# Performance work log

Measured on AMD Instinct MI355X. Metric: run time of the kernel, lower is better.

## Reference

```python
import jax, jax.numpy as jnp
import numpy as np
from jax import lax

B, CIN, H, W = 8, 3, 256, 256
CMID = 16          # conv out channels == config.in_channels
DM = 256           # d_model
P = 2              # patch size (hardcoded in Downsample)
DI = 512           # d_inner = expand * d_model
NH, HD, NS, KC = 8, 64, 128, 4   # heads, headdim, d_state, d_conv
CONVDIM = DI + 2 * NS            # 768
PROJ = 2 * DI + 2 * NS + NH      # 1288


def _sincos2d(dim, gs):
    # 2d sin-cos positional embedding, matches get_2d_sincos_pos_embed
    def emb1d(d, pos):
        omega = 1.0 / (10000.0 ** (jnp.arange(d // 2, dtype=jnp.float32) / (d / 2.0)))
        out = pos[:, None] * omega[None, :]
        return jnp.concatenate([jnp.sin(out), jnp.cos(out)], axis=1)
    g = jnp.arange(gs, dtype=jnp.float32)
    grid = jnp.stack(jnp.meshgrid(g, g), 0).reshape(2, -1)  # [2, gs*gs]
    return jnp.concatenate([emb1d(dim // 2, grid[0]), emb1d(dim // 2, grid[1])], 1)


def _mamba2(u, in_proj_w, conv1d_w, conv1d_b, dt_bias, A_log, D, norm_w, out_proj_w):
    b, l, _ = u.shape
    zxbcdt = jnp.einsum('bld,pd->blp', u, in_proj_w)              # [b,l,1288]
    z = zxbcdt[..., :DI]
    xBC = zxbcdt[..., DI:DI + CONVDIM]
    dt = zxbcdt[..., DI + CONVDIM:]                                # [b,l,NH]
    # causal depthwise conv1d over sequence, then SiLU
    xc = lax.conv_general_dilated(xBC.transpose(0, 2, 1), conv1d_w, (1,), [(KC - 1, 0)],
                                  feature_group_count=CONVDIM,
                                  dimension_numbers=('NCH', 'OIH', 'NCH'))
    xBC = jax.nn.silu(xc + conv1d_b[None, :, None]).transpose(0, 2, 1)
    xh = xBC[..., :DI].reshape(b, l, NH, HD)                       # [b,l,h,p]
    Bm = xBC[..., DI:DI + NS]                                      # [b,l,n]
    Cm = xBC[..., DI + NS:]                                        # [b,l,n]
    dt = jax.nn.softplus(dt + dt_bias)                             # [b,l,h]
    dA = jnp.exp(dt * (-jnp.exp(A_log)))                           # [b,l,h]
    dtx = dt[..., None] * xh                                       # [b,l,h,p]

    def step(s, inp):
        dtx_t, B_t, C_t, dA_t = inp
        s = s * dA_t[..., None, None] + dtx_t[..., None] * B_t[:, None, None, :]
        return s, jnp.einsum('bhpn,bn->bhp', s, C_t)

    s0 = jnp.zeros((b, NH, HD, NS), u.dtype)
    _, ys = lax.scan(step, s0, (dtx.transpose(1, 0, 2, 3), Bm.transpose(1, 0, 2),
                                Cm.transpose(1, 0, 2), dA.transpose(1, 0, 2)))
    y = ys.transpose(1, 0, 2, 3) + D[None, None, :, None] * xh     # [b,l,h,p]
    y = y.reshape(b, l, DI) * jax.nn.silu(z)                       # gated
    y = y * lax.rsqrt(jnp.mean(y * y, -1, keepdims=True) + 1e-5) * norm_w
    return jnp.einsum('bld,od->blo', y, out_proj_w)


def setup_inputs() -> dict:
    key = jax.random.key(0)
    ks = jax.random.split(key, 12)
    r = lambda i, s, sc: jax.random.normal(ks[i], s, jnp.float32) * sc
    return {
        'x': jax.random.normal(ks[0], (B, CIN, H, W), jnp.float32),
        'conv_w': r(1, (CMID, CIN, 3, 3), 0.1), 'conv_b': jnp.zeros((CMID,), jnp.float32),
        'bn_gamma': jnp.ones((CMID,), jnp.float32), 'bn_beta': jnp.zeros((CMID,), jnp.float32),
        'patch_w': r(2, (DM, CMID, P, P), 0.1), 'patch_b': jnp.zeros((DM,), jnp.float32),
        'in_proj_w': r(3, (PROJ, DM), 0.02),
        'conv1d_w': r(4, (CONVDIM, 1, KC), 0.1), 'conv1d_b': jnp.zeros((CONVDIM,), jnp.float32),
        'dt_bias': r(5, (NH,), 0.5),
        'A_log': jax.random.uniform(ks[6], (NH,), jnp.float32),
        'D': jnp.ones((NH,), jnp.float32),
        'norm_w': jnp.ones((DI,), jnp.float32),
        'out_proj_w': r(7, (DM, DI), 0.02),
        'final_w': r(8, (P * P * CMID, DM), 0.02), 'final_b': jnp.zeros((P * P * CMID,), jnp.float32),
    }


def reference(x, conv_w, conv_b, bn_gamma, bn_beta, patch_w, patch_b, in_proj_w,
              conv1d_w, conv1d_b, dt_bias, A_log, D, norm_w, out_proj_w, final_w, final_b):
    # Conv2d k=3 s=2 p=1 -> BatchNorm2d (training-mode batch stats) -> GELU
    h = lax.conv_general_dilated(x, conv_w, (2, 2), [(1, 1), (1, 1)],
                                 dimension_numbers=('NCHW', 'OIHW', 'NCHW')) + conv_b[None, :, None, None]
    mu = jnp.mean(h, (0, 2, 3), keepdims=True)
    var = jnp.var(h, (0, 2, 3), keepdims=True)
    h = (h - mu) * lax.rsqrt(var + 1e-5) * bn_gamma[None, :, None, None] + bn_beta[None, :, None, None]
    h = jax.nn.gelu(h, approximate=False)
    # PatchEmbed: conv k=p s=p, flatten to tokens, add frozen sincos pos embed
    t = lax.conv_general_dilated(h, patch_w, (P, P), 'VALID',
                                 dimension_numbers=('NCHW', 'OIHW', 'NCHW')) + patch_b[None, :, None, None]
    b, d, gh, gw = t.shape
    tok = t.reshape(b, d, gh * gw).transpose(0, 2, 1) + _sincos2d(DM, gh)[None]
    # MambaBlock: Mamba2(x) + x  (layers=1; repo loop discards all but last layer)
    y = _mamba2(tok, in_proj_w, conv1d_w, conv1d_b, dt_bias, A_log, D, norm_w, out_proj_w) + tok
    # FinalLayer: linear only (norm_final is unused in its forward)
    o = jnp.einsum('bld,od->blo', y, final_w) + final_b
    # unpatchify
    o = o.reshape(b, gh, gw, P, P, CMID)
    o = jnp.einsum('nhwpqc->nchpwq', o).reshape(b, CMID, gh * P, gw * P)
    return o
```

## Files before the change

### kernel.cpp

```cpp
#include <hip/hip_runtime.h>
#include <math.h>

#define B_  8
#define CIN 3
#define HIN 256
#define WIN 256
#define CMID 16
#define HMID 128
#define WMID 128
#define DM 256
#define L_ 4096
#define DI 512
#define NH 8
#define HD 64
#define NS 128
#define KC 4
#define CONVDIM 768
#define PROJ 1288
#define NPADIN 1408
#define MTOK (B_*L_)
#define QCH 128
#define NCH 32

typedef unsigned short bf16;
typedef __attribute__((ext_vector_type(8))) short bf16x8;
typedef __attribute__((ext_vector_type(4))) float f32x4;

__device__ inline float bf2f(bf16 u) { return __uint_as_float(((unsigned int)u) << 16); }
__device__ inline bf16 f2bf(float f) {
  unsigned int x = __float_as_uint(f);
  return (bf16)((x + 0x7fffu + ((x >> 16) & 1u)) >> 16);
}
__device__ inline unsigned int pack2bf(float a, float b) {
  return (unsigned int)f2bf(a) | ((unsigned int)f2bf(b) << 16);
}

__global__ void k_conv1(const float* __restrict__ x, const float* __restrict__ w,
                        const float* __restrict__ bias, float* __restrict__ out) {
  int idx = blockIdx.x*256 + threadIdx.x;
  if (idx >= B_*CMID*HMID*WMID) return;
  int xo = idx & 127, yo = (idx>>7)&127, co = (idx>>14)&15, b = idx>>18;
  float acc = bias[co];
  const float* xb = x + (size_t)b*CIN*HIN*WIN;
  const float* wc = w + co*CIN*9;
  #pragma unroll
  for (int ci=0; ci<CIN; ci++)
    #pragma unroll
    for (int ky=0; ky<3; ky++) {
      int yi = 2*yo - 1 + ky;
      if (yi < 0 || yi >= HIN) continue;
      #pragma unroll
      for (int kx=0; kx<3; kx++) {
        int xi = 2*xo - 1 + kx;
        if (xi < 0 || xi >= WIN) continue;
        acc += xb[(ci*HIN + yi)*WIN + xi] * wc[(ci*3+ky)*3+kx];
      }
    }
  out[idx] = acc;
}

__global__ __launch_bounds__(256) void k_bnstatsA(const float* __restrict__ h, float2* __restrict__ part) {
  int blk = blockIdx.x;
  const float4* base = (const float4*)(h + ((size_t)(blk>>2))*16384 + (blk&3)*4096);
  int tid = threadIdx.x;
  float s=0.f, s2=0.f;
  #pragma unroll
  for (int i=0;i<4;i++){
    float4 v = base[i*256 + tid];
    s += v.x+v.y+v.z+v.w;
    s2 += v.x*v.x + v.y*v.y + v.z*v.z + v.w*v.w;
  }
  #pragma unroll
  for (int off=1; off<64; off<<=1) { s += __shfl_xor(s, off); s2 += __shfl_xor(s2, off); }
  __shared__ float sb[2][4];
  if ((tid&63)==0){ sb[0][tid>>6]=s; sb[1][tid>>6]=s2; }
  __syncthreads();
  if (tid==0) part[blk] = make_float2(sb[0][0]+sb[0][1]+sb[0][2]+sb[0][3],
                                      sb[1][0]+sb[1][1]+sb[1][2]+sb[1][3]);
}

__global__ void k_bnstatsB(const float2* __restrict__ part, float* __restrict__ stats) {
  int lane = threadIdx.x;
  int c = lane >> 2, j0 = lane & 3;
  float s=0.f, s2=0.f;
  #pragma unroll
  for (int j=j0; j<32; j+=4){
    int b = j >> 2, chunk = j & 3;
    float2 p = part[(b*16+c)*4 + chunk];
    s += p.x; s2 += p.y;
  }
  s += __shfl_xor(s,1); s2 += __shfl_xor(s2,1);
  s += __shfl_xor(s,2); s2 += __shfl_xor(s2,2);
  if (j0==0){
    const float inv = 1.f/131072.f;
    float mean = s*inv;
    float var  = s2*inv - mean*mean;
    stats[c]      = mean;
    stats[16 + c] = rsqrtf(var + 1e-5f);
  }
}

__global__ __launch_bounds__(256) void k_patch(const float* __restrict__ h, const float* __restrict__ pw,
                       const float* __restrict__ pb, const float* __restrict__ stats,
                       const float* __restrict__ gamma, const float* __restrict__ beta,
                       bf16* __restrict__ tok) {
  int grp = blockIdx.x;
  int b = grp >> 9, g8 = grp & 511;
  int g0 = g8 << 3;
  int gy = g0 >> 6, gx0 = g0 & 63;
  __shared__ float sh[8][64];
  int tid = threadIdx.x;
  {
    int tk = tid >> 5, jj = (tid & 31)*2;
    int ci = jj >> 2, p = (jj >> 1) & 1;
    const float* src = &h[((size_t)(b*CMID+ci)*HMID + 2*gy+p)*WMID + 2*(gx0+tk)];
    float2 xv = *(const float2*)src;
    float mean = stats[ci], rstd = stats[16+ci];
    float sc = rstd*gamma[ci], be = beta[ci] - mean*sc;
    float v0 = xv.x*sc + be;
    float v1 = xv.y*sc + be;
    v0 = 0.5f*v0*(1.f + erff(v0*0.70710678118654752f));
    v1 = 0.5f*v1*(1.f + erff(v1*0.70710678118654752f));
    sh[tk][jj] = v0; sh[tk][jj+1] = v1;
  }
  __syncthreads();
  int d = tid;
  float wr[64];
  #pragma unroll
  for (int i4=0;i4<16;i4++) *(float4*)&wr[i4*4] = *(const float4*)&pw[d*64 + i4*4];
  float bias = pb[d];
  int i = d & 63;
  float omega = expf(-(float)i * (9.210340371976184f/64.f));
  #pragma unroll
  for (int tk=0;tk<8;tk++){
    float acc = bias;
    #pragma unroll
    for (int j=0;j<64;j++) acc = fmaf(sh[tk][j], wr[j], acc);
    float gv = (d < 128) ? (float)(gx0+tk) : (float)gy;
    float ph = gv * omega;
    float pos = (d & 64) ? __cosf(ph) : __sinf(ph);
    tok[((size_t)((b<<12) + g0 + tk))*DM + d] = f2bf(acc + pos);
  }
}

__global__ void k_cvtw(const float* __restrict__ src, bf16* __restrict__ dst,
                       int N, int kshift, int total) {
  int idx = blockIdx.x*256 + threadIdx.x;
  if (idx >= total) return;
  int n = idx >> kshift;
  dst[idx] = (n < N) ? f2bf(src[idx]) : (bf16)0;
}

template<int EPI>
__global__ __launch_bounds__(512) void k_mgemm(
    const bf16* __restrict__ A, const bf16* __restrict__ Bw, int K,
    bf16* __restrict__ o_z, bf16* __restrict__ o_x,
    bf16* __restrict__ o_y, const bf16* __restrict__ res,
    const float* __restrict__ dt_bias, const float* __restrict__ A_log,
    float* __restrict__ dtv, float* __restrict__ dAv,
    float* __restrict__ o_f, const float* __restrict__ fbias) {
  __shared__ __align__(16) char smem[49152];
  bf16* sA = (bf16*)smem;
  bf16* sB = (bf16*)(smem + 32768);
  bf16* sT = (bf16*)smem;
  int tid = threadIdx.x;
  int lane = tid & 63, wid = tid >> 6;
  int wr = wid >> 1, wc = wid & 1;
  int m0 = blockIdx.x*256, n0 = blockIdx.y*128;
  int nk = K >> 5;

  f32x4 acc[4][4];
  #pragma unroll
  for (int i=0;i<4;i++)
    #pragma unroll
    for (int j=0;j<4;j++)
      acc[i][j] = (f32x4){0.f,0.f,0.f,0.f};

  auto stage = [&](int buf, int ks){
    int kk = ks << 5;
    #pragma unroll
    for (int i=0;i<2;i++){
      int j = i*512 + tid;
      int row = j >> 2, cc = j & 3;
      int kg = cc ^ (row & 3);
      unsigned ldsoff = (unsigned)(buf*16384 + (i*512 + wid*64) * 16);
      __builtin_amdgcn_global_load_lds(
        (const __attribute__((address_space(1))) void*)(A + (size_t)(m0+row)*K + kk + kg*8),
        (__attribute__((address_space(3))) void*)((char*)sA + ldsoff), 16, 0, 0);
    }
    {
      int row = tid >> 2, cc = tid & 3;
      int kg = cc ^ (row & 3);
      unsigned ldsoff = (unsigned)(buf*8192 + (wid*64) * 16);
      __builtin_amdgcn_global_load_lds(
        (const __attribute__((address_space(1))) void*)(Bw + (size_t)(n0+row)*K + kk + kg*8),
        (__attribute__((address_space(3))) void*)((char*)sB + ldsoff), 16, 0, 0);
    }
  };

  int r = lane & 15, q = lane >> 4;
  int kgo = (q ^ (r & 3)) << 3;

  stage(0, 0);
  for (int ks=0; ks<nk; ++ks){
    int cur = ks & 1;
    __syncthreads();
    if (ks+1 < nk) stage(cur^1, ks+1);
    bf16x8 af[4], bfv[4];
    #pragma unroll
    for (int a=0;a<4;a++){
      int rown = wc*64 + a*16 + r;
      af[a] = *(const bf16x8*)&sB[cur*4096 + rown*32 + kgo];
    }
    #pragma unroll
    for (int bfr=0;bfr<4;bfr++){
      int rowm = wr*64 + bfr*16 + r;
      bfv[bfr] = *(const bf16x8*)&sA[cur*8192 + rowm*32 + kgo];
    }
    #pragma unroll
    for (int a=0;a<4;a++)
      #pragma unroll
      for (int bfr=0;bfr<4;bfr++)
        acc[a][bfr] = __builtin_amdgcn_mfma_f32_16x16x32_bf16(af[a], bfv[bfr], acc[a][bfr], 0, 0, 0);
  }

  if (EPI == 0 && n0 >= DI + CONVDIM) {
    #pragma unroll
    for (int a=0;a<4;a++){
      int n4 = n0 + wc*64 + a*16 + q*4;
      if (n4 >= PROJ) continue;
      #pragma unroll
      for (int bfr=0;bfr<4;bfr++){
        int m = m0 + wr*64 + bfr*16 + r;
        f32x4 v = acc[a][bfr];
        #pragma unroll
        for (int rr=0;rr<4;rr++){
          int hh = n4 + rr - (DI + CONVDIM);
          if (hh < NH){
            float xv = v[rr] + dt_bias[hh];
            float dt = (xv > 20.f) ? xv : log1pf(expf(xv));
            dtv[(size_t)m*NH + hh] = dt;
            dAv[(size_t)m*NH + hh] = expf(-expf(A_log[hh]) * dt);
          }
        }
      }
    }
    return;
  }
  if (EPI == 2) {
    #pragma unroll
    for (int a=0;a<4;a++){
      int n4 = n0 + wc*64 + a*16 + q*4;
      #pragma unroll
      for (int bfr=0;bfr<4;bfr++){
        int m = m0 + wr*64 + bfr*16 + r;
        f32x4 v = acc[a][bfr];
        #pragma unroll
        for (int rr=0;rr<4;rr++){
          int n = n4 + rr;
          if (n < 64) {
            float vv = v[rr] + fbias[n];
            int b = m >> 12, g = m & 4095;
            int gy = g >> 6, gx = g & 63;
            int p = n >> 5, qq = (n>>4)&1, cc2 = n & 15;
            o_f[(((size_t)(b*CMID+cc2))*HMID + 2*gy+p)*WMID + (2*gx+qq)] = vv;
          }
        }
      }
    }
    return;
  }

  #pragma unroll
  for (int h2=0; h2<2; ++h2){
    __syncthreads();
    if (wc == h2){
      #pragma unroll
      for (int a=0;a<4;a++){
        int nl = a*16 + q*4;
        #pragma unroll
        for (int bfr=0;bfr<4;bfr++){
          int ml = wr*64 + bfr*16 + r;
          f32x4 v = acc[a][bfr];
          *(uint2*)&sT[ml*72 + nl] = make_uint2(pack2bf(v[0],v[1]), pack2bf(v[2],v[3]));
        }
      }
    }
    __syncthreads();
    int ml = tid >> 1, ch = tid & 1;
    int m = m0 + ml;
    int ncol = n0 + h2*64 + ch*32;
    const bf16* src = &sT[ml*72 + ch*32];
    if (EPI == 0){
      bf16* dst = (n0 < DI) ? (o_z + (size_t)m*DI + ncol)
                            : (o_x + (size_t)m*CONVDIM + (ncol - DI));
      #pragma unroll
      for (int i4=0;i4<4;i4++)
        *(uint4*)(dst + i4*8) = *(const uint4*)(src + i4*8);
    } else {
      bf16* dst = o_y + (size_t)m*DM + ncol;
      const bf16* rsv = res + (size_t)m*DM + ncol;
      #pragma unroll
      for (int i4=0;i4<4;i4++){
        uint4 t = *(const uint4*)(src + i4*8);
        uint4 rv = *(const uint4*)(rsv + i4*8);
        unsigned tu[4]={t.x,t.y,t.z,t.w}, ru[4]={rv.x,rv.y,rv.z,rv.w};
        unsigned ou[4];
        #pragma unroll
        for (int k2=0;k2<4;k2++){
          float a0 = bf2f((bf16)(tu[k2]&0xffffu)) + bf2f((bf16)(ru[k2]&0xffffu));
          float a1 = bf2f((bf16)(tu[k2]>>16))     + bf2f((bf16)(ru[k2]>>16));
          ou[k2] = pack2bf(a0,a1);
        }
        *(uint4*)(dst + i4*8) = make_uint4(ou[0],ou[1],ou[2],ou[3]);
      }
    }
  }
}

__global__ __launch_bounds__(256) void k_conv1d(const bf16* __restrict__ xpre, const float* __restrict__ cw,
                         const float* __restrict__ cb, bf16* __restrict__ xbc) {
  int idx = blockIdx.x*256 + threadIdx.x;
  int gch = idx % 96;
  int tb  = idx / 96;
  int ch0 = gch*8;
  int bl0 = tb*8;
  int l0 = bl0 & (L_-1);
  float wv[32];
  #pragma unroll
  for (int i=0;i<8;i++) *(float4*)&wv[i*4] = *(const float4*)&cw[ch0*KC + i*4];
  float bs[8];
  *(float4*)&bs[0] = *(const float4*)&cb[ch0];
  *(float4*)&bs[4] = *(const float4*)&cb[ch0+4];
  uint4 rows[11];
  #pragma unroll
  for (int j=0;j<11;j++){
    int lk = l0 - 3 + j;
    if (lk < 0) rows[j] = make_uint4(0u,0u,0u,0u);
    else rows[j] = *(const uint4*)(xpre + ((size_t)bl0 - 3 + j)*CONVDIM + ch0);
  }
  #pragma unroll
  for (int t=0;t<8;t++){
    float acc[8];
    #pragma unroll
    for (int i=0;i<8;i++) acc[i] = bs[i];
    #pragma unroll
    for (int k=0;k<KC;k++){
      uint4 u = rows[t+k];
      unsigned uu[4]={u.x,u.y,u.z,u.w};
      #pragma unroll
      for (int c2=0;c2<4;c2++){
        float lo = __uint_as_float(uu[c2]<<16);
        float hi = __uint_as_float(uu[c2]&0xffff0000u);
        acc[c2*2]   = fmaf(wv[(c2*2)*4 + k],   lo, acc[c2*2]);
        acc[c2*2+1] = fmaf(wv[(c2*2+1)*4 + k], hi, acc[c2*2+1]);
      }
    }
    unsigned ou[4];
    #pragma unroll
    for (int c2=0;c2<4;c2++){
      float v0 = acc[c2*2], v1 = acc[c2*2+1];
      v0 = v0 / (1.f + __expf(-v0));
      v1 = v1 / (1.f + __expf(-v1));
      ou[c2] = pack2bf(v0, v1);
    }
    *(uint4*)(xbc + (size_t)(bl0+t)*CONVDIM + ch0) = make_uint4(ou[0],ou[1],ou[2],ou[3]);
  }
}

__global__ __launch_bounds__(512) void k_ssd1(const bf16* __restrict__ xbc,
    const float* __restrict__ dtv, const float* __restrict__ A_log,
    bf16* __restrict__ ys, bf16* __restrict__ Sst) {
  int blk = blockIdx.x;
  int c = blk & (NCH-1), h = (blk>>5)&7, b = blk>>8;
  int tid = threadIdx.x;
  int lane = tid & 63, wid = tid >> 6;
  int r = lane & 15, q = lane >> 4;
  size_t rowbase = (size_t)b*L_ + (size_t)c*QCH;
  float eA = __expf(A_log[h]);

  __shared__ __align__(16) char smem[81920];
  bf16* sB  = (bf16*)smem;
  bf16* sC  = (bf16*)(smem + 32768);
  bf16* sDX = (bf16*)(smem + 65536);
  float* fDT = (float*)(smem + 65536);
  float* fL  = fDT + 128;
  float* fWS = fL + 128;
  float* fWT = fWS + 128;

  #pragma unroll
  for (int i=0;i<8;i++){
    int id = i*512 + tid;
    int row = id >> 5, cg = id & 31;
    uint4 u = *(const uint4*)(xbc + (rowbase+row)*CONVDIM + DI + cg*8);
    if (cg < 16) *(uint4*)&sB[row*128 + ((cg ^ (row&15))<<3)] = u;
    else { int cg2 = cg-16; *(uint4*)&sC[row*128 + ((cg2 ^ (row&15))<<3)] = u; }
  }
  if (tid < 128) fDT[tid] = dtv[(rowbase+tid)*NH + h];
  __syncthreads();

  float inc = 0.f;
  if (tid < 128){
    inc = fDT[tid];
    #pragma unroll
    for (int off=1; off<64; off<<=1){
      float u = __shfl_up(inc, off);
      if (lane >= off) inc += u;
    }
    if (lane==63) fWT[wid] = inc;
  }
  __syncthreads();
  if (tid < 128){
    if (wid==1) inc += fWT[0];
    fL[tid] = inc;
  }

  int wr = wid >> 1, wc = wid & 1;
  f32x4 accG[2][4];
  #pragma unroll
  for (int i=0;i<2;i++)
    #pragma unroll
    for (int j=0;j<4;j++) accG[i][j] = (f32x4){0.f,0.f,0.f,0.f};
  #pragma unroll
  for (int ks=0; ks<4; ks++){
    bf16x8 af[2], bfv[4];
    #pragma unroll
    for (int mf=0;mf<2;mf++){
      int s = wr*32 + mf*16 + r;
      af[mf] = *(const bf16x8*)&sB[s*128 + (((ks*4+q) ^ (s&15))<<3)];
    }
    #pragma unroll
    for (int nf=0;nf<4;nf++){
      int t = wc*64 + nf*16 + r;
      bfv[nf] = *(const bf16x8*)&sC[t*128 + (((ks*4+q) ^ (t&15))<<3)];
    }
    #pragma unroll
    for (int mf=0;mf<2;mf++)
      #pragma unroll
      for (int nf=0;nf<4;nf++)
        accG[mf][nf] = __builtin_amdgcn_mfma_f32_16x16x32_bf16(af[mf], bfv[nf], accG[mf][nf], 0, 0, 0);
  }
  __syncthreads();

  bf16* sW = sC;
  #pragma unroll
  for (int mf=0;mf<2;mf++){
    int sb4 = wr*32 + mf*16 + q*4;
    int cb4 = sb4 >> 3, se4 = sb4 & 7;
    #pragma unroll
    for (int nf=0;nf<4;nf++){
      int t = wc*64 + nf*16 + r;
      float Lt = fL[t];
      float w[4];
      #pragma unroll
      for (int rr=0;rr<4;rr++){
        int s = sb4 + rr;
        float v = 0.f;
        if (s <= t) v = accG[mf][nf][rr] * fDT[s] * __expf(-eA*(Lt - fL[s]));
        w[rr] = v;
      }
      *(uint2*)&sW[t*128 + ((cb4 ^ (t&15))<<3) + se4] =
          make_uint2(pack2bf(w[0],w[1]), pack2bf(w[2],w[3]));
    }
  }
  if (tid < 128) fWS[tid] = fDT[tid]*__expf(-eA*(fL[127]-fL[tid]));
  __syncthreads();

  int nT = tid >> 2, sg = tid & 3;
  unsigned short vals[32];
  #pragma unroll
  for (int i8=0;i8<4;i8++){
    #pragma unroll
    for (int j=0;j<8;j++){
      int s = sg*32 + i8*8 + j;
      float bv = bf2f(sB[s*128 + (((nT>>3) ^ (s&15))<<3) + (nT&7)]);
      vals[i8*8+j] = f2bf(bv * fWS[s]);
    }
  }
  __syncthreads();

  #pragma unroll
  for (int i8=0;i8<4;i8++){
    int s8 = sg*4 + i8;
    *(uint4*)&sB[nT*128 + ((s8 ^ (nT&15))<<3)] = *(const uint4*)&vals[i8*8];
  }
  {
    int s0 = (tid >> 3)*2;
    int p0 = (tid & 7)*8;
    const bf16* x0 = xbc + (rowbase+s0)*CONVDIM + h*HD + p0;
    uint4 u0 = *(const uint4*)x0;
    uint4 u1 = *(const uint4*)(x0 + CONVDIM);
    unsigned a0[4]={u0.x,u0.y,u0.z,u0.w}, a1[4]={u1.x,u1.y,u1.z,u1.w};
    int cb2 = s0 >> 3, se = s0 & 7;
    #pragma unroll
    for (int jp=0;jp<4;jp++){
      unsigned w0=a0[jp], w1=a1[jp];
      unsigned lo = (w0 & 0xffffu) | (w1 << 16);
      unsigned hi = (w0 >> 16) | (w1 & 0xffff0000u);
      int pA = p0 + jp*2, pB = pA+1;
      *(unsigned*)&sDX[pA*128 + ((cb2 ^ (pA&15))<<3) + se] = lo;
      *(unsigned*)&sDX[pB*128 + ((cb2 ^ (pB&15))<<3) + se] = hi;
    }
  }
  __syncthreads();

  {
    int wrp = wid >> 2, wct = wid & 3;
    f32x4 acc2[2][2];
    #pragma unroll
    for (int i=0;i<2;i++){ acc2[i][0]=(f32x4){0.f,0.f,0.f,0.f}; acc2[i][1]=(f32x4){0.f,0.f,0.f,0.f}; }
    #pragma unroll
    for (int ks=0; ks<4; ks++){
      bf16x8 af[2], bfv[2];
      #pragma unroll
      for (int mf=0;mf<2;mf++){
        int p = wrp*32 + mf*16 + r;
        af[mf] = *(const bf16x8*)&sDX[p*128 + (((ks*4+q) ^ (p&15))<<3)];
      }
      #pragma unroll
      for (int nf=0;nf<2;nf++){
        int t = wct*32 + nf*16 + r;
        bfv[nf] = *(const bf16x8*)&sW[t*128 + (((ks*4+q) ^ (t&15))<<3)];
      }
      #pragma unroll
      for (int mf=0;mf<2;mf++)
        #pragma unroll
        for (int nf=0;nf<2;nf++)
          acc2[mf][nf] = __builtin_amdgcn_mfma_f32_16x16x32_bf16(af[mf], bfv[nf], acc2[mf][nf], 0, 0, 0);
    }
    #pragma unroll
    for (int mf=0;mf<2;mf++){
      int pb = wrp*32 + mf*16 + q*4;
      #pragma unroll
      for (int nf=0;nf<2;nf++){
        int t = wct*32 + nf*16 + r;
        f32x4 v = acc2[mf][nf];
        *(uint2*)(ys + (rowbase+t)*DI + h*HD + pb) =
            make_uint2(pack2bf(v[0],v[1]), pack2bf(v[2],v[3]));
      }
    }
  }
  {
    int wrn = wid >> 1, wcp = wid & 1;
    f32x4 acc3[2][2];
    #pragma unroll
    for (int i=0;i<2;i++){ acc3[i][0]=(f32x4){0.f,0.f,0.f,0.f}; acc3[i][1]=(f32x4){0.f,0.f,0.f,0.f}; }
    #pragma unroll
    for (int ks=0; ks<4; ks++){
      bf16x8 af[2], bfv[2];
      #pragma unroll
      for (int mf=0;mf<2;mf++){
        int n = wrn*32 + mf*16 + r;
        af[mf] = *(const bf16x8*)&sB[n*128 + (((ks*4+q) ^ (n&15))<<3)];
      }
      #pragma unroll
      for (int nf=0;nf<2;nf++){
        int p = wcp*32 + nf*16 + r;
        bfv[nf] = *(const bf16x8*)&sDX[p*128 + (((ks*4+q) ^ (p&15))<<3)];
      }
      #pragma unroll
      for (int mf=0;mf<2;mf++)
        #pragma unroll
        for (int nf=0;nf<2;nf++)
          acc3[mf][nf] = __builtin_amdgcn_mfma_f32_16x16x32_bf16(af[mf], bfv[nf], acc3[mf][nf], 0, 0, 0);
    }
    size_t sb = (((size_t)(b*NH+h))*NCH + c)*8192;
    #pragma unroll
    for (int mf=0;mf<2;mf++){
      int nb = wrn*32 + mf*16 + q*4;
      #pragma unroll
      for (int nf=0;nf<2;nf++){
        int p = wcp*32 + nf*16 + r;
        f32x4 v = acc3[mf][nf];
        *(uint2*)(Sst + sb + (size_t)p*128 + nb) =
            make_uint2(pack2bf(v[0],v[1]), pack2bf(v[2],v[3]));
      }
    }
  }
}

template<int NCHT, int QCHT>
__global__ __launch_bounds__(256) void k_scan2(bf16* __restrict__ Sst, const float* __restrict__ dAv) {
  constexpr int SEG = QCHT/16;
  int blk = blockIdx.x;
  int bh = blk>>2, q = blk&3;
  int b = bh>>3, h = bh&7;
  int tid = threadIdx.x;
  __shared__ float sP[NCHT];
  {
    int c = tid / SEG, seg = tid & (SEG-1);
    float prod = 1.f;
    size_t base = ((size_t)b*L_ + c*QCHT + seg*16)*NH + h;
    #pragma unroll
    for (int k=0;k<16;k++) prod *= dAv[base + (size_t)k*NH];
    #pragma unroll
    for (int off=1; off<SEG; off<<=1) prod *= __shfl_xor(prod, off);
    if (seg==0) sP[c] = prod;
  }
  __syncthreads();
  int e0 = q*2048 + tid*8;
  float acc[8];
  #pragma unroll
  for (int j=0;j<8;j++) acc[j]=0.f;
  size_t sbase = (size_t)bh*NCHT*8192 + e0;
  for (int c=0;c<NCHT;c++){
    bf16* ptr = Sst + sbase + (size_t)c*8192;
    uint4 u = *(const uint4*)ptr;
    unsigned int uu[4] = {u.x,u.y,u.z,u.w};
    float tv[8];
    #pragma unroll
    for (int k=0;k<4;k++){
      tv[2*k]   = __uint_as_float(uu[k]<<16);
      tv[2*k+1] = __uint_as_float(uu[k]&0xffff0000u);
    }
    uint4 o;
    o.x = pack2bf(acc[0],acc[1]); o.y = pack2bf(acc[2],acc[3]);
    o.z = pack2bf(acc[4],acc[5]); o.w = pack2bf(acc[6],acc[7]);
    asm volatile("s_waitcnt vmcnt(0)" ::: "memory");
    *(uint4*)ptr = o;
    float P = sP[c];
    #pragma unroll
    for (int j=0;j<8;j++) acc[j] = tv[j] + P*acc[j];
  }
}

__global__ __launch_bounds__(256) void k_ssd3(const bf16* __restrict__ xbc,
    const float* __restrict__ dtv, const float* __restrict__ A_log,
    const bf16* __restrict__ Sst, bf16* __restrict__ ys) {
  int blk = blockIdx.x;
  int c = blk & (NCH-1), h = (blk>>5)&7, b = blk>>8;
  int tid = threadIdx.x;
  int lane = tid & 63, wid = tid >> 6;
  int r = lane & 15, q = lane >> 4;
  size_t rowbase = (size_t)b*L_ + (size_t)c*QCH;
  float eA = __expf(A_log[h]);

  __shared__ __align__(16) bf16 sC[128*128];
  __shared__ float sDT[128];
  __shared__ float sAt[128];
  __shared__ float sWT[2];

  #pragma unroll
  for (int i=0;i<8;i++){
    int id = i*256 + tid;
    int row = id >> 4, cg = id & 15;
    uint4 u = *(const uint4*)(xbc + (rowbase+row)*CONVDIM + DI + NS + cg*8);
    *(uint4*)&sC[row*128 + ((cg ^ (row&15))<<3)] = u;
  }
  if (tid < 128) sDT[tid] = dtv[(rowbase+tid)*NH + h];
  __syncthreads();
  float inc = 0.f;
  if (tid < 128){
    inc = sDT[tid];
    #pragma unroll
    for (int off=1; off<64; off<<=1){
      float u = __shfl_up(inc, off);
      if (lane >= off) inc += u;
    }
    if (lane==63) sWT[wid] = inc;
  }
  __syncthreads();
  if (tid < 128){
    if (wid==1) inc += sWT[0];
    sAt[tid] = __expf(-eA*inc);
  }
  __syncthreads();

  int wrp = wid >> 1, wct = wid & 1;
  size_t sb = (((size_t)(b*NH+h))*NCH + c)*8192;
  f32x4 accP[2][4];
  #pragma unroll
  for (int i=0;i<2;i++)
    #pragma unroll
    for (int j=0;j<4;j++) accP[i][j] = (f32x4){0.f,0.f,0.f,0.f};
  #pragma unroll
  for (int ks=0; ks<4; ks++){
    bf16x8 af[2], bfv[4];
    #pragma unroll
    for (int mf=0;mf<2;mf++){
      int p = wrp*32 + mf*16 + r;
      af[mf] = *(const bf16x8*)(Sst + sb + (size_t)p*128 + ks*32 + q*8);
    }
    #pragma unroll
    for (int nf=0;nf<4;nf++){
      int t = wct*64 + nf*16 + r;
      bfv[nf] = *(const bf16x8*)&sC[t*128 + (((ks*4+q) ^ (t&15))<<3)];
    }
    #pragma unroll
    for (int mf=0;mf<2;mf++)
      #pragma unroll
      for (int nf=0;nf<4;nf++)
        accP[mf][nf] = __builtin_amdgcn_mfma_f32_16x16x32_bf16(af[mf], bfv[nf], accP[mf][nf], 0, 0, 0);
  }
  #pragma unroll
  for (int mf=0;mf<2;mf++){
    int pb = wrp*32 + mf*16 + q*4;
    #pragma unroll
    for (int nf=0;nf<4;nf++){
      int t = wct*64 + nf*16 + r;
      float at = sAt[t];
      bf16* yp = ys + (rowbase+t)*DI + h*HD + pb;
      uint2 old = *(uint2*)yp;
      float o0 = bf2f((bf16)(old.x & 0xffffu))  + at*accP[mf][nf][0];
      float o1 = bf2f((bf16)(old.x >> 16))      + at*accP[mf][nf][1];
      float o2 = bf2f((bf16)(old.y & 0xffffu))  + at*accP[mf][nf][2];
      float o3 = bf2f((bf16)(old.y >> 16))      + at*accP[mf][nf][3];
      *(uint2*)yp = make_uint2(pack2bf(o0,o1), pack2bf(o2,o3));
    }
  }
}

__global__ __launch_bounds__(256) void k_combine(bf16* __restrict__ ys, const bf16* __restrict__ xbc,
                         const bf16* __restrict__ z, const float* __restrict__ Dp,
                         const float* __restrict__ nw) {
  int bl = blockIdx.x;
  int tid = threadIdx.x;
  bf16* yrow = ys + (size_t)bl*DI;
  const bf16* xrow = xbc + (size_t)bl*CONVDIM;
  const bf16* zrow = z + (size_t)bl*DI;
  float v[2]; float ss = 0.f;
  #pragma unroll
  for (int i=0;i<2;i++) {
    int d = tid + i*256;
    float xh = bf2f(xrow[d]);
    float y = bf2f(yrow[d]) + Dp[d>>6]*xh;
    float zv = bf2f(zrow[d]);
    y *= zv / (1.f + expf(-zv));
    v[i] = y; ss += y*y;
  }
  #pragma unroll
  for (int off=1; off<64; off<<=1) ss += __shfl_xor(ss, off);
  __shared__ float sb[4];
  if ((tid&63)==0) sb[tid>>6]=ss;
  __syncthreads();
  float total = sb[0]+sb[1]+sb[2]+sb[3];
  float scale = rsqrtf(total * (1.f/512.f) + 1e-5f);
  #pragma unroll
  for (int i=0;i<2;i++) {
    int d = tid + i*256;
    yrow[d] = f2bf(v[i]*scale*nw[d]);
  }
}

extern "C" void kernel_launch(void* const* d_in, const int* in_sizes, int n_in,
                              void* d_out, int out_size, void* d_ws, size_t ws_size,
                              hipStream_t stream) {
  const float* x         = (const float*)d_in[0];
  const float* conv_w    = (const float*)d_in[1];
  const float* conv_b    = (const float*)d_in[2];
  const float* bn_gamma  = (const float*)d_in[3];
  const float* bn_beta   = (const float*)d_in[4];
  const float* patch_w   = (const float*)d_in[5];
  const float* patch_b   = (const float*)d_in[6];
  const float* in_proj_w = (const float*)d_in[7];
  const float* conv1d_w  = (const float*)d_in[8];
  const float* conv1d_b  = (const float*)d_in[9];
  const float* dt_bias   = (const float*)d_in[10];
  const float* A_log     = (const float*)d_in[11];
  const float* Dp        = (const float*)d_in[12];
  const float* norm_w    = (const float*)d_in[13];
  const float* out_proj_w= (const float*)d_in[14];
  const float* final_w   = (const float*)d_in[15];
  const float* final_b   = (const float*)d_in[16];
  float* out = (float*)d_out;

  char* Wb = (char*)d_ws;
  float* h_buf = (float*)(Wb + 0);
  bf16*  winb  = (bf16*)(Wb + 0);
  bf16*  woutb = (bf16*)(Wb + 0);
  bf16*  wfinb = (bf16*)(Wb + 262144);
  bf16*  xpost = (bf16*)(Wb + 0);
  float2* part = (float2*)(Wb + 50331648);
  bf16*  tok   = (bf16*)(Wb + 50331648);
  bf16*  zbuf  = (bf16*)(Wb + 67108864);
  bf16*  y2b   = (bf16*)(Wb + 67108864);
  bf16*  xpre  = (bf16*)(Wb + 100663296);
  bf16*  ysb   = (bf16*)(Wb + 100663296);
  bf16*  Sst   = (bf16*)(Wb + 134217728);
  float* dtv   = (float*)(Wb + 134217728 + 33554432);
  float* dAv   = dtv + 262144;
  float* stats = dAv + 262144;
  const size_t NEED = 134217728ull + 33554432 + 2097152 + 256;
  if (ws_size < NEED) {
    hipMemsetAsync(d_out, 0, (size_t)out_size*sizeof(float), stream);
    return;
  }

  k_conv1<<<dim3((B_*CMID*HMID*WMID)/256), dim3(256), 0, stream>>>(x, conv_w, conv_b, h_buf);
  k_bnstatsA<<<dim3(512), dim3(256), 0, stream>>>(h_buf, part);
  k_bnstatsB<<<dim3(1), dim3(64), 0, stream>>>(part, stats);
  k_patch<<<dim3(MTOK/8), dim3(256), 0, stream>>>(h_buf, patch_w, patch_b, stats, bn_gamma, bn_beta, tok);
  k_cvtw<<<dim3((NPADIN*DM)/256), dim3(256), 0, stream>>>(in_proj_w, winb, PROJ, 8, NPADIN*DM);
  k_mgemm<0><<<dim3(MTOK/256, NPADIN/128), dim3(512), 0, stream>>>(tok, winb, DM,
      zbuf, xpre, nullptr, nullptr, dt_bias, A_log, dtv, dAv, nullptr, nullptr);
  k_conv1d<<<dim3((MTOK/8*96)/256), dim3(256), 0, stream>>>(xpre, conv1d_w, conv1d_b, xpost);
  k_ssd1<<<dim3(B_*NH*NCH), dim3(512), 0, stream>>>(xpost, dtv, A_log, ysb, Sst);
  k_scan2<NCH,QCH><<<dim3(B_*NH*4), dim3(256), 0, stream>>>(Sst, dAv);
  k_ssd3<<<dim3(B_*NH*NCH), dim3(256), 0, stream>>>(xpost, dtv, A_log, Sst, ysb);
  k_combine<<<dim3(MTOK), dim3(256), 0, stream>>>(ysb, xpost, zbuf, Dp, norm_w);
  k_cvtw<<<dim3((DM*DI)/256), dim3(256), 0, stream>>>(out_proj_w, woutb, DM, 9, DM*DI);
  k_cvtw<<<dim3((128*DM)/256), dim3(256), 0, stream>>>(final_w, wfinb, 64, 8, 128*DM);
  k_mgemm<1><<<dim3(MTOK/256, DM/128), dim3(512), 0, stream>>>(ysb, woutb, DI,
      nullptr, nullptr, y2b, tok, nullptr, nullptr, nullptr, nullptr, nullptr, nullptr);
  k_mgemm<2><<<dim3(MTOK/256, 1), dim3(512), 0, stream>>>(y2b, wfinb, DM,
      nullptr, nullptr, nullptr, nullptr, nullptr, nullptr, nullptr, nullptr, out, final_b);
}
```

Before: 336.9 us.

## Fuse out_proj GEMM, residual add and final linear into one kernel

Replaces the two back-to-back GEMM launches (out_proj with residual, then the final 256->64 linear with unpatchify scatter) with one kernel. Each block computes a 128-row by 256-column out_proj tile, adds the residual, stages the bf16 result in swizzled LDS, and runs the final linear from LDS. This avoids writing and re-reading the 32768x256 intermediate y2b and saves a launch. In exchange it uses a new 128-row tiling with one N-tile per block, which gives fewer and larger blocks (256 blocks), and the final weights are read directly from global memory.

```diff
diff --git a/kernel.cpp b/kernel.cpp
--- a/kernel.cpp
+++ b/kernel.cpp
@@ -247,29 +247,6 @@
     }
     return;
   }
-  if (EPI == 2) {
-    #pragma unroll
-    for (int a=0;a<4;a++){
-      int n4 = n0 + wc*64 + a*16 + q*4;
-      #pragma unroll
-      for (int bfr=0;bfr<4;bfr++){
-        int m = m0 + wr*64 + bfr*16 + r;
-        f32x4 v = acc[a][bfr];
-        #pragma unroll
-        for (int rr=0;rr<4;rr++){
-          int n = n4 + rr;
-          if (n < 64) {
-            float vv = v[rr] + fbias[n];
-            int b = m >> 12, g = m & 4095;
-            int gy = g >> 6, gx = g & 63;
-            int p = n >> 5, qq = (n>>4)&1, cc2 = n & 15;
-            o_f[(((size_t)(b*CMID+cc2))*HMID + 2*gy+p)*WMID + (2*gx+qq)] = vv;
-          }
-        }
-      }
-    }
-    return;
-  }
 
   #pragma unroll
   for (int h2=0; h2<2; ++h2){
@@ -291,29 +268,139 @@
     int m = m0 + ml;
     int ncol = n0 + h2*64 + ch*32;
     const bf16* src = &sT[ml*72 + ch*32];
-    if (EPI == 0){
-      bf16* dst = (n0 < DI) ? (o_z + (size_t)m*DI + ncol)
-                            : (o_x + (size_t)m*CONVDIM + (ncol - DI));
-      #pragma unroll
-      for (int i4=0;i4<4;i4++)
-        *(uint4*)(dst + i4*8) = *(const uint4*)(src + i4*8);
-    } else {
-      bf16* dst = o_y + (size_t)m*DM + ncol;
-      const bf16* rsv = res + (size_t)m*DM + ncol;
-      #pragma unroll
-      for (int i4=0;i4<4;i4++){
-        uint4 t = *(const uint4*)(src + i4*8);
-        uint4 rv = *(const uint4*)(rsv + i4*8);
-        unsigned tu[4]={t.x,t.y,t.z,t.w}, ru[4]={rv.x,rv.y,rv.z,rv.w};
-        unsigned ou[4];
+    bf16* dst = (n0 < DI) ? (o_z + (size_t)m*DI + ncol)
+                          : (o_x + (size_t)m*CONVDIM + (ncol - DI));
+    #pragma unroll
+    for (int i4=0;i4<4;i4++)
+      *(uint4*)(dst + i4*8) = *(const uint4*)(src + i4*8);
+  }
+}
+
+__global__ __launch_bounds__(512) void k_mgemm12(
+    const bf16* __restrict__ A, const bf16* __restrict__ Bw,
+    const bf16* __restrict__ res, const bf16* __restrict__ wfin,
+    const float* __restrict__ fbias, float* __restrict__ o_f) {
+  __shared__ __align__(16) char smem[49152];
+  bf16* sA = (bf16*)smem;
+  bf16* sB = (bf16*)(smem + 16384);
+  bf16* sY = (bf16*)smem;
+  int tid = threadIdx.x;
+  int lane = tid & 63, wid = tid >> 6;
+  int wr = wid >> 2, wc = wid & 3;
+  int m0 = blockIdx.x*128;
+  const int K = DI;
+  int nk = K >> 5;
+
+  f32x4 acc[4][4];
+  #pragma unroll
+  for (int i=0;i<4;i++)
+    #pragma unroll
+    for (int j=0;j<4;j++)
+      acc[i][j] = (f32x4){0.f,0.f,0.f,0.f};
+
+  auto stage = [&](int buf, int ks){
+    int kk = ks << 5;
+    {
+      int row = tid >> 2, cc = tid & 3;
+      int kg = cc ^ (row & 3);
+      unsigned ldsoff = (unsigned)(buf*8192 + (wid*64) * 16);
+      __builtin_amdgcn_global_load_lds(
+        (const __attribute__((address_space(1))) void*)(A + (size_t)(m0+row)*K + kk + kg*8),
+        (__attribute__((address_space(3))) void*)((char*)sA + ldsoff), 16, 0, 0);
+    }
+    #pragma unroll
+    for (int i=0;i<2;i++){
+      int j = i*512 + tid;
+      int row = j >> 2, cc = j & 3;
+      int kg = cc ^ (row & 3);
+      unsigned ldsoff = (unsigned)(buf*16384 + (i*512 + wid*64) * 16);
+      __builtin_amdgcn_global_load_lds(
+        (const __attribute__((address_space(1))) void*)(Bw + (size_t)row*K + kk + kg*8),
+        (__attribute__((address_space(3))) void*)((char*)sB + ldsoff), 16, 0, 0);
+    }
+  };
+
+  int r = lane & 15, q = lane >> 4;
+  int kgo = (q ^ (r & 3)) << 3;
+
+  stage(0, 0);
+  for (int ks=0; ks<nk; ++ks){
+    int cur = ks & 1;
+    __syncthreads();
+    if (ks+1 < nk) stage(cur^1, ks+1);
+    bf16x8 af[4], bfv[4];
+    #pragma unroll
+    for (int a=0;a<4;a++){
+      int rown = wc*64 + a*16 + r;
+      af[a] = *(const bf16x8*)&sB[cur*8192 + rown*32 + kgo];
+    }
+    #pragma unroll
+    for (int mf=0;mf<4;mf++){
+      int rowm = wr*64 + mf*16 + r;
+      bfv[mf] = *(const bf16x8*)&sA[cur*4096 + rowm*32 + kgo];
+    }
+    #pragma unroll
+    for (int a=0;a<4;a++)
+      #pragma unroll
+      for (int mf=0;mf<4;mf++)
+        acc[a][mf] = __builtin_amdgcn_mfma_f32_16x16x32_bf16(af[a], bfv[mf], acc[a][mf], 0, 0, 0);
+  }
+
+  f32x4 acc2[4];
+  #pragma unroll
+  for (int i=0;i<4;i++) acc2[i] = (f32x4){0.f,0.f,0.f,0.f};
+  int orow = wc*16 + r;
+
+  #pragma unroll
+  for (int j=0;j<4;j++){
+    __syncthreads();
+    if (wc == j){
+      #pragma unroll
+      for (int a=0;a<4;a++){
+        int kl = a*16 + q*4;
+        int chunk = kl >> 3, sub = (q & 1)*4;
         #pragma unroll
-        for (int k2=0;k2<4;k2++){
-          float a0 = bf2f((bf16)(tu[k2]&0xffffu)) + bf2f((bf16)(ru[k2]&0xffffu));
-          float a1 = bf2f((bf16)(tu[k2]>>16))     + bf2f((bf16)(ru[k2]>>16));
-          ou[k2] = pack2bf(a0,a1);
+        for (int mf=0;mf<4;mf++){
+          int ml = wr*64 + mf*16 + r;
+          int m = m0 + ml;
+          int n4 = wc*64 + kl;
+          uint2 rv = *(const uint2*)(res + (size_t)m*DM + n4);
+          f32x4 v = acc[a][mf];
+          float y0 = v[0] + bf2f((bf16)(rv.x & 0xffffu));
+          float y1 = v[1] + bf2f((bf16)(rv.x >> 16));
+          float y2 = v[2] + bf2f((bf16)(rv.y & 0xffffu));
+          float y3 = v[3] + bf2f((bf16)(rv.y >> 16));
+          *(uint2*)&sY[ml*64 + ((chunk ^ (ml&7))<<3) + sub] =
+              make_uint2(pack2bf(y0,y1), pack2bf(y2,y3));
         }
-        *(uint4*)(dst + i4*8) = make_uint4(ou[0],ou[1],ou[2],ou[3]);
-      }
+      }
+    }
+    __syncthreads();
+    #pragma unroll
+    for (int kstep=0;kstep<2;kstep++){
+      bf16x8 af2 = *(const bf16x8*)(wfin + (size_t)orow*DM + j*64 + kstep*32 + q*8);
+      #pragma unroll
+      for (int mf=0;mf<4;mf++){
+        int ml = wr*64 + mf*16 + r;
+        int cg = kstep*4 + q;
+        bf16x8 bv = *(const bf16x8*)&sY[ml*64 + ((cg ^ (ml&7))<<3)];
+        acc2[mf] = __builtin_amdgcn_mfma_f32_16x16x32_bf16(af2, bv, acc2[mf], 0, 0, 0);
+      }
+    }
+  }
+
+  #pragma unroll
+  for (int mf=0;mf<4;mf++){
+    int m = m0 + wr*64 + mf*16 + r;
+    int b = m >> 12, g = m & 4095;
+    int gy = g >> 6, gx = g & 63;
+    f32x4 v = acc2[mf];
+    #pragma unroll
+    for (int rr=0;rr<4;rr++){
+      int o = wc*16 + q*4 + rr;
+      float vv = v[rr] + fbias[o];
+      int p = o >> 5, qq = (o>>4)&1, cc2 = o & 15;
+      o_f[(((size_t)(b*CMID+cc2))*HMID + 2*gy+p)*WMID + (2*gx+qq)] = vv;
     }
   }
 }
@@ -773,7 +860,6 @@
   float2* part = (float2*)(Wb + 50331648);
   bf16*  tok   = (bf16*)(Wb + 50331648);
   bf16*  zbuf  = (bf16*)(Wb + 67108864);
-  bf16*  y2b   = (bf16*)(Wb + 67108864);
   bf16*  xpre  = (bf16*)(Wb + 100663296);
   bf16*  ysb   = (bf16*)(Wb + 100663296);
   bf16*  Sst   = (bf16*)(Wb + 134217728);
@@ -800,8 +886,5 @@
   k_combine<<<dim3(MTOK), dim3(256), 0, stream>>>(ysb, xpost, zbuf, Dp, norm_w);
   k_cvtw<<<dim3((DM*DI)/256), dim3(256), 0, stream>>>(out_proj_w, woutb, DM, 9, DM*DI);
   k_cvtw<<<dim3((128*DM)/256), dim3(256), 0, stream>>>(final_w, wfinb, 64, 8, 128*DM);
-  k_mgemm<1><<<dim3(MTOK/256, DM/128), dim3(512), 0, stream>>>(ysb, woutb, DI,
-      nullptr, nullptr, y2b, tok, nullptr, nullptr, nullptr, nullptr, nullptr, nullptr);
-  k_mgemm<2><<<dim3(MTOK/256, 1), dim3(512), 0, stream>>>(y2b, wfinb, DM,
-      nullptr, nullptr, nullptr, nullptr, nullptr, nullptr, nullptr, nullptr, out, final_b);
-}
+  k_mgemm12<<<dim3(MTOK/128), dim3(512), 0, stream>>>(ysb, woutb, tok, wfinb, final_b, out);
+}
```

Result: faster. 324.6 us (-3.7%).
